# Performance work log

Measured on AMD Instinct MI355X. Metric: run time of the kernel, lower is better.

Reference implementation:

```python
import jax, jax.numpy as jnp
import numpy as np

DYNAMIC_RANGE = 16  # from init_kwargs
MAX_VAL = 2 ** (DYNAMIC_RANGE - 1) - 1   # 32767
MIN_VAL = -(2 ** (DYNAMIC_RANGE - 1))    # -32768


def setup_inputs() -> dict:
    key = jax.random.key(0)
    k_img, k_w = jax.random.split(key)
    Z, Y, X = 128, 512, 512
    P = 15                      # prediction_bands
    image = jax.random.normal(k_img, (Z, Y, X), dtype=jnp.float32) * 100.0
    # weights buffer is [num_bands, 4 + prediction_bands]; original inits to zeros
    # (degenerate output), so we use small random weights in [-1, 1].
    weights = jax.random.normal(k_w, (Z, 4 + P), dtype=jnp.float32) * 0.05
    return {"image": image, "weights": weights}


def reference(image, weights):
    # image: [Z, Y, X], weights: [Z, 4 + P]
    Z, Y, X = image.shape
    P = weights.shape[1] - 4

    # Note: sample_representatives[z] = predictions[z] + residuals[z] = image[z],
    # so all neighbor extraction operates on the raw image. Weight updates in the
    # original only touch weights[z] AFTER band z is predicted and that row is
    # never read again, so the output depends only on the initial weights.

    # Spatial neighbors (zero-padded): N, W, NW, (N+W+NW)/3  -> [Z, Y, X, 4]
    pad = jnp.pad(image, ((0, 0), (1, 1), (1, 1)))
    north = pad[:, :-2, 1:-1]
    west = pad[:, 1:-1, :-2]
    northwest = pad[:, :-2, :-2]
    fourth = (north + west + northwest) / 3
    spatial = jnp.stack([north, west, northwest, fourth], axis=-1)

    # Spectral neighbors: bands z-P .. z-1, zero-padded at the front.
    # spec_pad[z + p] == image[z - P + p] (or 0 if out of range) -> [P, Z, Y, X]
    spec_pad = jnp.concatenate(
        [jnp.zeros((P, Y, X), dtype=image.dtype), image], axis=0)
    spectral = jnp.stack([spec_pad[p:p + Z] for p in range(P)], axis=0)

    # Per-band weighted sum over the 4 + P predictors, then clamp.
    pred = (jnp.einsum('zyxs,zs->zyx', spatial, weights[:, :4])
            + jnp.einsum('pzyx,zp->zyx', spectral, weights[:, 4:]))
    pred = jnp.clip(pred, MIN_VAL, MAX_VAL)

    residuals = image - pred
    return pred, residuals
```

## Files before the change

kernel.cpp:

```cpp
#include <hip/hip_runtime.h>

#define Zdim 128
#define Ydim 512
#define Xdim 512
#define Pdim 15
#define NWt  19
#define CHUNK 32

typedef __attribute__((ext_vector_type(4))) float f4;
struct F4 { float v[4]; };

__device__ __forceinline__ F4 ld4(const float* p) {
    f4 t = *(const f4*)p;
    F4 r; r.v[0] = t[0]; r.v[1] = t[1]; r.v[2] = t[2]; r.v[3] = t[3];
    return r;
}

__global__ __launch_bounds__(256, 4) void spec_pred_kernel(
    const float* __restrict__ img,
    const float* __restrict__ wts,
    float* __restrict__ out)
{
    const int bid = blockIdx.x;
    const int zc  = bid >> 8;
    const int r8  = bid & 255;
    const int yb  = ((r8 & 7) << 5) | (r8 >> 3);
    const int id  = (yb << 8) | threadIdx.x;
    const int xg  = (id & 127) << 2;
    const int y   = id >> 7;

    const unsigned plane = (unsigned)Ydim * Xdim;
    const unsigned pix   = (unsigned)y * Xdim + xg;
    const float* ip = img + pix;
    float* pp = out + pix;
    float* rp = out + (unsigned)Zdim * plane + pix;

    const int  z0 = zc * CHUNK;
    const bool hn = (y > 0);
    const bool hw = (xg > 0);
    const bool l0 = (threadIdx.x & 63) == 0;

    F4 h[Pdim];
    if (z0 == 0) {
#pragma unroll
        for (int p = 0; p < Pdim; ++p) h[p] = F4{{0, 0, 0, 0}};
    } else {
#pragma unroll
        for (int p = 0; p < Pdim; ++p)
            h[p] = ld4(ip + (unsigned)(z0 - Pdim + p) * plane);
    }

    F4 cb[3], nb[3];
    float wb[3], qb[3];

    auto LOAD = [&](int z, int b) {
        const float* p0 = ip + (unsigned)z * plane;
        cb[b] = ld4(p0);
        nb[b] = hn ? ld4(p0 - Xdim) : F4{{0, 0, 0, 0}};
        wb[b] = (l0 && hw)       ? p0[-1]        : 0.0f;
        qb[b] = (l0 && hw && hn) ? p0[-Xdim - 1] : 0.0f;
    };

    auto STEP = [&](int z, int b) {
        const float* wz = wts + z * NWt;
        const float w3 = wz[3] * (1.0f / 3.0f);
        const float a0 = wz[0] + w3, a1 = wz[1] + w3, a2 = wz[2] + w3;
        float we = __shfl_up(cb[b].v[3], 1);
        float qw = __shfl_up(nb[b].v[3], 1);
        if (l0) { we = wb[b]; qw = qb[b]; }
        f4 pv, rv;
#pragma unroll
        for (int e = 0; e < 4; ++e) {
            const float vn = nb[b].v[e];
            float a = wz[4] * h[0].v[e];
#pragma unroll
            for (int p = 1; p < Pdim; ++p) a = fmaf(wz[4 + p], h[p].v[e], a);
            a = fmaf(a0, vn, a);
            a = fmaf(a1, e ? cb[b].v[e - 1] : we, a);
            a = fmaf(a2, e ? nb[b].v[e - 1] : qw, a);
            a = fminf(fmaxf(a, -32768.0f), 32767.0f);
            pv[e] = a;
            rv[e] = cb[b].v[e] - a;
        }
        __builtin_nontemporal_store(pv, (f4*)(pp + (unsigned)z * plane));
        __builtin_nontemporal_store(rv, (f4*)(rp + (unsigned)z * plane));
#pragma unroll
        for (int p = 0; p < Pdim - 1; ++p) h[p] = h[p + 1];
        h[Pdim - 1] = cb[b];
    };

    LOAD(z0 + 0, 0);
    LOAD(z0 + 1, 1);
#pragma unroll 15
    for (int i = 0; i < CHUNK - 2; ++i) {
        LOAD(z0 + i + 2, (i + 2) % 3);
        STEP(z0 + i, i % 3);
    }
    STEP(z0 + CHUNK - 2, (CHUNK - 2) % 3);
    STEP(z0 + CHUNK - 1, (CHUNK - 1) % 3);
}

extern "C" void kernel_launch(void* const* d_in, const int* in_sizes, int n_in,
                              void* d_out, int out_size, void* d_ws, size_t ws_size,
                              hipStream_t stream) {
    const float* img = (const float*)d_in[0];
    const float* wts = (const float*)d_in[1];
    float* out = (float*)d_out;

    const int grid = 256 * (Zdim / CHUNK);
    spec_pred_kernel<<<grid, 256, 0, stream>>>(img, wts, out);
}
```

Measured before the change: 74.47 us.

## Process full Z column per thread, dropping z-chunk split and halo reloads

Each thread now walks all 128 bands instead of a 32-band chunk, so the grid shrinks to 256 blocks. This removes the redundant reload of the 15 preceding spectral planes that each chunk needed to seed its history registers. In exchange the launch has far fewer waves per CU, which reduces memory-latency hiding and parallelism. Launch bounds are relaxed to allow more registers.

Result: slower. 76.97 us (+3.4%).

```diff
diff --git a/kernel.cpp b/kernel.cpp
--- a/kernel.cpp
+++ b/kernel.cpp
@@ -5,7 +5,6 @@
 #define Xdim 512
 #define Pdim 15
 #define NWt  19
-#define CHUNK 32
 
 typedef __attribute__((ext_vector_type(4))) float f4;
 struct F4 { float v[4]; };
@@ -16,15 +15,13 @@
     return r;
 }
 
-__global__ __launch_bounds__(256, 4) void spec_pred_kernel(
+__global__ __launch_bounds__(256, 1) void spec_pred_kernel(
     const float* __restrict__ img,
     const float* __restrict__ wts,
     float* __restrict__ out)
 {
     const int bid = blockIdx.x;
-    const int zc  = bid >> 8;
-    const int r8  = bid & 255;
-    const int yb  = ((r8 & 7) << 5) | (r8 >> 3);
+    const int yb  = ((bid & 7) << 5) | (bid >> 3);
     const int id  = (yb << 8) | threadIdx.x;
     const int xg  = (id & 127) << 2;
     const int y   = id >> 7;
@@ -35,20 +32,13 @@
     float* pp = out + pix;
     float* rp = out + (unsigned)Zdim * plane + pix;
 
-    const int  z0 = zc * CHUNK;
     const bool hn = (y > 0);
     const bool hw = (xg > 0);
     const bool l0 = (threadIdx.x & 63) == 0;
 
     F4 h[Pdim];
-    if (z0 == 0) {
 #pragma unroll
-        for (int p = 0; p < Pdim; ++p) h[p] = F4{{0, 0, 0, 0}};
-    } else {
-#pragma unroll
-        for (int p = 0; p < Pdim; ++p)
-            h[p] = ld4(ip + (unsigned)(z0 - Pdim + p) * plane);
-    }
+    for (int p = 0; p < Pdim; ++p) h[p] = F4{{0, 0, 0, 0}};
 
     F4 cb[3], nb[3];
     float wb[3], qb[3];
@@ -89,15 +79,21 @@
         h[Pdim - 1] = cb[b];
     };
 
-    LOAD(z0 + 0, 0);
-    LOAD(z0 + 1, 1);
+    LOAD(0, 0);
+    LOAD(1, 1);
 #pragma unroll 15
-    for (int i = 0; i < CHUNK - 2; ++i) {
-        LOAD(z0 + i + 2, (i + 2) % 3);
-        STEP(z0 + i, i % 3);
+    for (int i = 0; i < 120; ++i) {
+        LOAD(i + 2, (i + 2) % 3);
+        STEP(i, i % 3);
     }
-    STEP(z0 + CHUNK - 2, (CHUNK - 2) % 3);
-    STEP(z0 + CHUNK - 1, (CHUNK - 1) % 3);
+    LOAD(122, 2); STEP(120, 0);
+    LOAD(123, 0); STEP(121, 1);
+    LOAD(124, 1); STEP(122, 2);
+    LOAD(125, 2); STEP(123, 0);
+    LOAD(126, 0); STEP(124, 1);
+    LOAD(127, 1); STEP(125, 2);
+    STEP(126, 0);
+    STEP(127, 1);
 }
 
 extern "C" void kernel_launch(void* const* d_in, const int* in_sizes, int n_in,
@@ -107,6 +103,5 @@
     const float* wts = (const float*)d_in[1];
     float* out = (float*)d_out;
 
-    const int grid = 256 * (Zdim / CHUNK);
-    spec_pred_kernel<<<grid, 256, 0, stream>>>(img, wts, out);
+    spec_pred_kernel<<<256, 256, 0, stream>>>(img, wts, out);
 }
```
